# Performance work log

Hardware: AMD Instinct MI355X
Metric: run time of the kernel (lower is better)

The kernel has to match this reference:

```python
import jax, jax.numpy as jnp
import numpy as np

# NOTE: in the original SelfAttention.forward, the selected/softmaxed/dropped
# attention `attn` is NEVER used: the output is `torch.matmul(attn_cont, value)`
# with the RAW pre-mask, pre-softmax, unscaled scores. The AutoSelectAttention /
# softmax / dropout branch is dead code w.r.t. the module output, so the faithful
# forward is out = proj_out( (Q K^T) V ) per head.

B, M, HID, K = 2, 2048, 1024, 16
D = HID // K


def setup_inputs() -> dict:
    key = jax.random.key(0)
    ks = jax.random.split(key, 6)
    s = 1.0 / np.sqrt(HID)
    return {
        "h": jax.random.normal(ks[0], (B, M, HID), jnp.float32),
        "Wq": jax.random.normal(ks[1], (HID, HID), jnp.float32) * s,
        "Wk": jax.random.normal(ks[2], (HID, HID), jnp.float32) * s,
        "Wv": jax.random.normal(ks[3], (HID, HID), jnp.float32) * s,
        "Wspan": jax.random.normal(ks[4], (2 * K, HID), jnp.float32) * s,
        "Wo": jax.random.normal(ks[5], (HID, HID), jnp.float32) * s,
    }


def _heads(x, d):
    # [B, M, K*d] -> [B, K, M, d]
    b, m, _ = x.shape
    return x.reshape(b, m, K, d).transpose(0, 2, 1, 3)


def reference(h, Wq, Wk, Wv, Wspan, Wo):
    # torch Linear: y = x @ W.T  (weights stored [out, in])
    q = _heads(h @ Wq.T, D)          # [B,K,M,D]
    k = _heads(h @ Wk.T, D)          # [B,K,M,D]
    v = _heads(h @ Wv.T, D)          # [B,K,M,D]
    span = _heads(h @ Wspan.T, 2)    # [B,K,M,2] -- dead code in original, kept for parity
    del span
    # raw scores (attn_cont in the original)
    scores = jnp.einsum("bkmd,bknd->bkmn", q, k)      # [B,K,M,M]
    # original: out = attn_cont @ value (select/softmax branch unused)
    out = jnp.einsum("bkmn,bknd->bkmd", scores, v)    # [B,K,M,D]
    out = out.transpose(0, 2, 1, 3).reshape(B, M, HID)
    return out @ Wo.T
```

## Files before the change

### kernel.cpp

```cpp
#include <hip/hip_runtime.h>
#include <hip/hip_bf16.h>
#include <stdint.h>

typedef __hip_bfloat16 bf16_t;
typedef __attribute__((ext_vector_type(8))) __bf16 bf16x8;
typedef __attribute__((ext_vector_type(4))) float floatx4;

#define BM 128
#define BN 128
#define BK 64

__device__ inline void async_load16(const void* g, void* l) {
  __builtin_amdgcn_global_load_lds(
      (const __attribute__((address_space(1))) unsigned int*)g,
      (__attribute__((address_space(3))) unsigned int*)l,
      16, 0, 0);
}

__device__ inline void unpack8_bf16(float* dst, uint4 u) {
  const unsigned w[4] = {u.x, u.y, u.z, u.w};
#pragma unroll
  for (int p = 0; p < 4; ++p) {
    dst[2 * p]     = __uint_as_float(w[p] << 16);
    dst[2 * p + 1] = __uint_as_float(w[p] & 0xffff0000u);
  }
}

__device__ inline unsigned short bf16_bits(float f) {
  bf16_t b = __float2bfloat16(f);
  return *(const unsigned short*)&b;
}

__global__ void cvt_one(const float* __restrict__ src, bf16_t* __restrict__ dst) {
  const int i = (blockIdx.x * 256 + threadIdx.x) * 4;
  float4 f = *(const float4*)(src + i);
  union { unsigned short u[4]; uint2 v; } p;
  p.u[0] = bf16_bits(f.x); p.u[1] = bf16_bits(f.y);
  p.u[2] = bf16_bits(f.z); p.u[3] = bf16_bits(f.w);
  *(uint2*)(dst + i) = p.v;
}

__global__ void cvt_w4(const float* __restrict__ s0, const float* __restrict__ s1,
                       const float* __restrict__ s2, const float* __restrict__ s3,
                       bf16_t* __restrict__ d0, bf16_t* __restrict__ d1,
                       bf16_t* __restrict__ d2, bf16_t* __restrict__ d3) {
  const float* s; bf16_t* d;
  switch (blockIdx.y) {
    case 0: s = s0; d = d0; break;
    case 1: s = s1; d = d1; break;
    case 2: s = s2; d = d2; break;
    default: s = s3; d = d3; break;
  }
  const int i = (blockIdx.x * 256 + threadIdx.x) * 4;
  float4 f = *(const float4*)(s + i);
  union { unsigned short u[4]; uint2 v; } p;
  p.u[0] = bf16_bits(f.x); p.u[1] = bf16_bits(f.y);
  p.u[2] = bf16_bits(f.z); p.u[3] = bf16_bits(f.w);
  *(uint2*)(d + i) = p.v;
}

template <typename OutT>
__global__ __launch_bounds__(256, 2)
void gemm_nt(const bf16_t* __restrict__ A, int lda,
             const bf16_t* __restrict__ B0, const bf16_t* __restrict__ B1,
             const bf16_t* __restrict__ B2,
             OutT* __restrict__ C, int ldc, int Kdim)
{
  __shared__ alignas(16) __bf16 As[BM * BK];
  __shared__ alignas(16) __bf16 Bs[BN * BK];

  const int t = threadIdx.x;
  const int lane = t & 63;
  const int wave = t >> 6;
  const int wm = wave >> 1;
  const int wn = wave & 1;

  const int m0 = blockIdx.x * BM;
  const int nblk = blockIdx.y * BN;
  const int mat = nblk >> 10;
  const bf16_t* __restrict__ B = (mat == 0) ? B0 : ((mat == 1) ? B1 : B2);
  const int n0 = nblk & 1023;

  floatx4 acc[4][4];
#pragma unroll
  for (int i = 0; i < 4; ++i)
#pragma unroll
    for (int j = 0; j < 4; ++j)
      acc[i][j] = (floatx4){0.f, 0.f, 0.f, 0.f};

  const int srow = t >> 3;
  const int sgs = t & 7;

  for (int k0 = 0; k0 < Kdim; k0 += BK) {
#pragma unroll
    for (int r4 = 0; r4 < 4; ++r4) {
      const int row = r4 * 32 + srow;
      const int gsrc = sgs ^ (row & 7);
      async_load16(A + (size_t)(m0 + row) * lda + k0 + gsrc * 8,
                   &As[row * BK + sgs * 8]);
      async_load16(B + (size_t)(n0 + row) * Kdim + k0 + gsrc * 8,
                   &Bs[row * BK + sgs * 8]);
    }
    __syncthreads();
#pragma unroll
    for (int ks = 0; ks < 2; ++ks) {
      bf16x8 af[4], bfv[4];
#pragma unroll
      for (int i = 0; i < 4; ++i) {
        const int row = wm * 64 + i * 16 + (lane & 15);
        const int g = ks * 4 + (lane >> 4);
        af[i] = *(const bf16x8*)&As[row * BK + (g ^ (row & 7)) * 8];
      }
#pragma unroll
      for (int j = 0; j < 4; ++j) {
        const int row = wn * 64 + j * 16 + (lane & 15);
        const int g = ks * 4 + (lane >> 4);
        bfv[j] = *(const bf16x8*)&Bs[row * BK + (g ^ (row & 7)) * 8];
      }
#pragma unroll
      for (int i = 0; i < 4; ++i)
#pragma unroll
        for (int j = 0; j < 4; ++j)
          acc[i][j] = __builtin_amdgcn_mfma_f32_16x16x32_bf16(
              af[i], bfv[j], acc[i][j], 0, 0, 0);
    }
    __syncthreads();
  }

  const int ccol = lane & 15;
  const int crow = (lane >> 4) * 4;
#pragma unroll
  for (int i = 0; i < 4; ++i) {
#pragma unroll
    for (int j = 0; j < 4; ++j) {
      const int gcol = nblk + wn * 64 + j * 16 + ccol;
      const int growb = m0 + wm * 64 + i * 16 + crow;
#pragma unroll
      for (int r = 0; r < 4; ++r) {
        float v = acc[i][j][r];
        if constexpr (__is_same(OutT, bf16_t))
          C[(size_t)(growb + r) * ldc + gcol] = __float2bfloat16(v);
        else
          C[(size_t)(growb + r) * ldc + gcol] = v;
      }
    }
  }
}

__global__ __launch_bounds__(256)
void ktv_kernel(const bf16_t* __restrict__ qkv, float* __restrict__ S)
{
  __shared__ float Kf[32][64];
  __shared__ float Vf[32][64];
  const int bh = blockIdx.x;
  const int b = bh >> 4, hh = bh & 15;
  const int mc = blockIdx.y;
  const int t = threadIdx.x;
  const int d0 = (t & 15) * 4;
  const int e0 = (t >> 4) * 4;

  const bf16_t* kbase = qkv + (size_t)b * 2048 * 3072 + 1024 + hh * 64;
  const bf16_t* vbase = kbase + 1024;

  float acc[4][4];
#pragma unroll
  for (int i = 0; i < 4; ++i)
#pragma unroll
    for (int j = 0; j < 4; ++j) acc[i][j] = 0.f;

  const int sr = t >> 3;
  const int sc = (t & 7) * 8;

  for (int m0 = mc * 256; m0 < mc * 256 + 256; m0 += 32) {
    uint4 ku = *(const uint4*)(kbase + (size_t)(m0 + sr) * 3072 + sc);
    uint4 vu = *(const uint4*)(vbase + (size_t)(m0 + sr) * 3072 + sc);
    __syncthreads();
    unpack8_bf16(&Kf[sr][sc], ku);
    unpack8_bf16(&Vf[sr][sc], vu);
    __syncthreads();
#pragma unroll
    for (int m = 0; m < 32; ++m) {
      float kv[4], vv[4];
#pragma unroll
      for (int i = 0; i < 4; ++i) kv[i] = Kf[m][d0 + i];
#pragma unroll
      for (int j = 0; j < 4; ++j) vv[j] = Vf[m][e0 + j];
#pragma unroll
      for (int i = 0; i < 4; ++i)
#pragma unroll
        for (int j = 0; j < 4; ++j) acc[i][j] += kv[i] * vv[j];
    }
  }
  float* Sp = S + (size_t)bh * 64 * 64;
#pragma unroll
  for (int i = 0; i < 4; ++i)
#pragma unroll
    for (int j = 0; j < 4; ++j)
      atomicAdd(&Sp[(d0 + i) * 64 + e0 + j], acc[i][j]);
}

__global__ __launch_bounds__(256)
void qs_kernel(const bf16_t* __restrict__ qkv, const float* __restrict__ S,
               bf16_t* __restrict__ O)
{
  __shared__ float Ss[64][64];
  const int bh = blockIdx.x;
  const int b = bh >> 4, hh = bh & 15;
  const int mt = blockIdx.y;
  const int t = threadIdx.x;

  const float* Sp = S + (size_t)bh * 4096;
  {
    float* sf = &Ss[0][0];
#pragma unroll
    for (int i = 0; i < 16; ++i) sf[t * 16 + i] = Sp[t * 16 + i];
  }
  __syncthreads();

  const int row = t >> 1;
  const int e0 = (t & 1) * 32;
  const int m = mt * 128 + row;
  const bf16_t* qp = qkv + (size_t)(b * 2048 + m) * 3072 + hh * 64;

  float acc[32];
#pragma unroll
  for (int e = 0; e < 32; ++e) acc[e] = 0.f;

  const uint4* qv = (const uint4*)qp;
#pragma unroll
  for (int c = 0; c < 8; ++c) {
    float qf[8];
    unpack8_bf16(qf, qv[c]);
#pragma unroll
    for (int p = 0; p < 8; ++p) {
      const int d = c * 8 + p;
      const float q = qf[p];
#pragma unroll
      for (int e = 0; e < 32; ++e) acc[e] += q * Ss[d][e0 + e];
    }
  }

  bf16_t* op = O + (size_t)(b * 2048 + m) * 3072 + hh * 64 + e0;
#pragma unroll
  for (int c = 0; c < 4; ++c) {
    uint4 u;
    unsigned* pu = (unsigned*)&u;
#pragma unroll
    for (int p = 0; p < 4; ++p) {
      const int e = c * 8 + p * 2;
      unsigned lo = bf16_bits(acc[e]);
      unsigned hi = bf16_bits(acc[e + 1]);
      pu[p] = lo | (hi << 16);
    }
    ((uint4*)op)[c] = u;
  }
}

extern "C" void kernel_launch(void* const* d_in, const int* in_sizes, int n_in,
                              void* d_out, int out_size, void* d_ws, size_t ws_size,
                              hipStream_t stream)
{
  const float* h  = (const float*)d_in[0];
  const float* Wq = (const float*)d_in[1];
  const float* Wk = (const float*)d_in[2];
  const float* Wv = (const float*)d_in[3];
  const float* Wo = (const float*)d_in[5];
  float* out = (float*)d_out;

  char* ws = (char*)d_ws;
  bf16_t* hb  = (bf16_t*)(ws);
  bf16_t* Wqb = (bf16_t*)(ws + (8u << 20));
  bf16_t* Wkb = (bf16_t*)(ws + (10u << 20));
  bf16_t* Wvb = (bf16_t*)(ws + (12u << 20));
  bf16_t* Wob = (bf16_t*)(ws + (14u << 20));
  bf16_t* qkv = (bf16_t*)(ws + (16u << 20));
  float*  S   = (float*) (ws + (40u << 20));

  hipMemsetAsync(S, 0, 32 * 64 * 64 * sizeof(float), stream);

  cvt_one<<<dim3(4096), 256, 0, stream>>>(h, hb);
  cvt_w4<<<dim3(1024, 4), 256, 0, stream>>>(Wq, Wk, Wv, Wo, Wqb, Wkb, Wvb, Wob);

  gemm_nt<bf16_t><<<dim3(32, 24), 256, 0, stream>>>(hb, 1024, Wqb, Wkb, Wvb, qkv, 3072, 1024);
  ktv_kernel<<<dim3(32, 8), 256, 0, stream>>>(qkv, S);
  qs_kernel<<<dim3(32, 16), 256, 0, stream>>>(qkv, S, qkv + 1024);
  gemm_nt<float><<<dim3(32, 8), 256, 0, stream>>>(qkv + 1024, 3072, Wob, Wob, Wob, out, 1024, 1024);
}
```

Before: 176.6 us.

## Merge conversion kernels, add 8-wave output GEMM, split KtV reduction finer

The two fp32-to-bf16 conversion kernels become a single launch that dispatches on block index. The QKV GEMM's launch bounds are raised to 3 blocks per CU. The K^T V reduction is split into twice as many row chunks for more blocks. The output projection now uses a dedicated 512-thread GEMM in which each wave owns a 32x64 sub-tile, giving more waves per tile. This cuts launch overhead and increases parallelism, but it may add register pressure in the QKV GEMM and more atomic contention in the reduction.

```diff
diff --git a/kernel.cpp b/kernel.cpp
--- a/kernel.cpp
+++ b/kernel.cpp
@@ -31,27 +31,21 @@
   return *(const unsigned short*)&b;
 }
 
-__global__ void cvt_one(const float* __restrict__ src, bf16_t* __restrict__ dst) {
-  const int i = (blockIdx.x * 256 + threadIdx.x) * 4;
-  float4 f = *(const float4*)(src + i);
-  union { unsigned short u[4]; uint2 v; } p;
-  p.u[0] = bf16_bits(f.x); p.u[1] = bf16_bits(f.y);
-  p.u[2] = bf16_bits(f.z); p.u[3] = bf16_bits(f.w);
-  *(uint2*)(dst + i) = p.v;
-}
-
-__global__ void cvt_w4(const float* __restrict__ s0, const float* __restrict__ s1,
-                       const float* __restrict__ s2, const float* __restrict__ s3,
-                       bf16_t* __restrict__ d0, bf16_t* __restrict__ d1,
-                       bf16_t* __restrict__ d2, bf16_t* __restrict__ d3) {
-  const float* s; bf16_t* d;
-  switch (blockIdx.y) {
-    case 0: s = s0; d = d0; break;
-    case 1: s = s1; d = d1; break;
-    case 2: s = s2; d = d2; break;
-    default: s = s3; d = d3; break;
-  }
-  const int i = (blockIdx.x * 256 + threadIdx.x) * 4;
+__global__ void cvt_all(const float* __restrict__ h, const float* __restrict__ Wq,
+                        const float* __restrict__ Wk, const float* __restrict__ Wv,
+                        const float* __restrict__ Wo,
+                        bf16_t* __restrict__ hb, bf16_t* __restrict__ Wqb,
+                        bf16_t* __restrict__ Wkb, bf16_t* __restrict__ Wvb,
+                        bf16_t* __restrict__ Wob)
+{
+  const int bid = blockIdx.x;
+  const float* s; bf16_t* d; int base;
+  if (bid < 4096)      { s = h;  d = hb;  base = bid; }
+  else if (bid < 5120) { s = Wq; d = Wqb; base = bid - 4096; }
+  else if (bid < 6144) { s = Wk; d = Wkb; base = bid - 5120; }
+  else if (bid < 7168) { s = Wv; d = Wvb; base = bid - 6144; }
+  else                 { s = Wo; d = Wob; base = bid - 7168; }
+  const int i = (base * 256 + threadIdx.x) * 4;
   float4 f = *(const float4*)(s + i);
   union { unsigned short u[4]; uint2 v; } p;
   p.u[0] = bf16_bits(f.x); p.u[1] = bf16_bits(f.y);
@@ -59,12 +53,11 @@
   *(uint2*)(d + i) = p.v;
 }
 
-template <typename OutT>
-__global__ __launch_bounds__(256, 2)
+__global__ __launch_bounds__(256, 3)
 void gemm_nt(const bf16_t* __restrict__ A, int lda,
              const bf16_t* __restrict__ B0, const bf16_t* __restrict__ B1,
              const bf16_t* __restrict__ B2,
-             OutT* __restrict__ C, int ldc, int Kdim)
+             bf16_t* __restrict__ C, int ldc, int Kdim)
 {
   __shared__ alignas(16) __bf16 As[BM * BK];
   __shared__ alignas(16) __bf16 Bs[BN * BK];
@@ -136,13 +129,86 @@
       const int gcol = nblk + wn * 64 + j * 16 + ccol;
       const int growb = m0 + wm * 64 + i * 16 + crow;
 #pragma unroll
-      for (int r = 0; r < 4; ++r) {
-        float v = acc[i][j][r];
-        if constexpr (__is_same(OutT, bf16_t))
-          C[(size_t)(growb + r) * ldc + gcol] = __float2bfloat16(v);
-        else
-          C[(size_t)(growb + r) * ldc + gcol] = v;
+      for (int r = 0; r < 4; ++r)
+        C[(size_t)(growb + r) * ldc + gcol] = __float2bfloat16(acc[i][j][r]);
+    }
+  }
+}
+
+__global__ __launch_bounds__(512, 2)
+void gemm_nt8(const bf16_t* __restrict__ A, int lda,
+              const bf16_t* __restrict__ B,
+              float* __restrict__ C, int ldc, int Kdim)
+{
+  __shared__ alignas(16) __bf16 As[BM * BK];
+  __shared__ alignas(16) __bf16 Bs[BN * BK];
+
+  const int t = threadIdx.x;
+  const int lane = t & 63;
+  const int wave = t >> 6;
+  const int wm = wave >> 1;
+  const int wn = wave & 1;
+
+  const int m0 = blockIdx.x * BM;
+  const int n0 = blockIdx.y * BN;
+
+  floatx4 acc[2][4];
+#pragma unroll
+  for (int i = 0; i < 2; ++i)
+#pragma unroll
+    for (int j = 0; j < 4; ++j)
+      acc[i][j] = (floatx4){0.f, 0.f, 0.f, 0.f};
+
+  const int srow = t >> 3;
+  const int sgs = t & 7;
+
+  for (int k0 = 0; k0 < Kdim; k0 += BK) {
+#pragma unroll
+    for (int r2 = 0; r2 < 2; ++r2) {
+      const int row = r2 * 64 + srow;
+      const int gsrc = sgs ^ (row & 7);
+      async_load16(A + (size_t)(m0 + row) * lda + k0 + gsrc * 8,
+                   &As[row * BK + sgs * 8]);
+      async_load16(B + (size_t)(n0 + row) * Kdim + k0 + gsrc * 8,
+                   &Bs[row * BK + sgs * 8]);
+    }
+    __syncthreads();
+#pragma unroll
+    for (int ks = 0; ks < 2; ++ks) {
+      bf16x8 af[2], bfv[4];
+#pragma unroll
+      for (int i = 0; i < 2; ++i) {
+        const int row = wm * 32 + i * 16 + (lane & 15);
+        const int g = ks * 4 + (lane >> 4);
+        af[i] = *(const bf16x8*)&As[row * BK + (g ^ (row & 7)) * 8];
       }
+#pragma unroll
+      for (int j = 0; j < 4; ++j) {
+        const int row = wn * 64 + j * 16 + (lane & 15);
+        const int g = ks * 4 + (lane >> 4);
+        bfv[j] = *(const bf16x8*)&Bs[row * BK + (g ^ (row & 7)) * 8];
+      }
+#pragma unroll
+      for (int i = 0; i < 2; ++i)
+#pragma unroll
+        for (int j = 0; j < 4; ++j)
+          acc[i][j] = __builtin_amdgcn_mfma_f32_16x16x32_bf16(
+              af[i], bfv[j], acc[i][j], 0, 0, 0);
+    }
+    __syncthreads();
+  }
+
+  const int ccol = lane & 15;
+  const int crow = (lane >> 4) * 4;
+#pragma unroll
+  for (int i = 0; i < 2; ++i) {
+#pragma unroll
+    for (int j = 0; j < 4; ++j) {
+      const int gcol = n0 + wn * 64 + j * 16 + ccol;
+      const int growb = m0 + wm * 32 + i * 16 + crow;
+#pragma unroll
+      for (int r = 0; r < 4; ++r)
+        C[(size_t)(growb + r) * ldc + gcol] = acc[i][j][r];
     }
   }
 }
@@ -171,7 +237,7 @@
   const int sr = t >> 3;
   const int sc = (t & 7) * 8;
 
-  for (int m0 = mc * 256; m0 < mc * 256 + 256; m0 += 32) {
+  for (int m0 = mc * 128; m0 < mc * 128 + 128; m0 += 32) {
     uint4 ku = *(const uint4*)(kbase + (size_t)(m0 + sr) * 3072 + sc);
     uint4 vu = *(const uint4*)(vbase + (size_t)(m0 + sr) * 3072 + sc);
     __syncthreads();
@@ -278,11 +344,10 @@
 
   hipMemsetAsync(S, 0, 32 * 64 * 64 * sizeof(float), stream);
 
-  cvt_one<<<dim3(4096), 256, 0, stream>>>(h, hb);
-  cvt_w4<<<dim3(1024, 4), 256, 0, stream>>>(Wq, Wk, Wv, Wo, Wqb, Wkb, Wvb, Wob);
-
-  gemm_nt<bf16_t><<<dim3(32, 24), 256, 0, stream>>>(hb, 1024, Wqb, Wkb, Wvb, qkv, 3072, 1024);
-  ktv_kernel<<<dim3(32, 8), 256, 0, stream>>>(qkv, S);
+  cvt_all<<<dim3(8192), 256, 0, stream>>>(h, Wq, Wk, Wv, Wo, hb, Wqb, Wkb, Wvb, Wob);
+
+  gemm_nt<<<dim3(32, 24), 256, 0, stream>>>(hb, 1024, Wqb, Wkb, Wvb, qkv, 3072, 1024);
+  ktv_kernel<<<dim3(32, 16), 256, 0, stream>>>(qkv, S);
   qs_kernel<<<dim3(32, 16), 256, 0, stream>>>(qkv, S, qkv + 1024);
-  gemm_nt<float><<<dim3(32, 8), 256, 0, stream>>>(qkv + 1024, 3072, Wob, Wob, Wob, out, 1024, 1024);
-}
+  gemm_nt8<<<dim3(32, 8), 512, 0, stream>>>(qkv + 1024, 3072, Wob, out, 1024, 1024);
+}
```

After: 186.4 us. 5.6% more time.
